# Kernel optimization log

Measured on AMD Instinct MI355X. Metric: run time of the kernel, lower is better.

Reference implementation:

```python
import jax, jax.numpy as jnp
import numpy as np

N, K = 10000, 32          # nodes, max neighbors
NUM_ELEM = 100
D_ATOM = 128              # atom embedding size
D_DIR_IN, D_DIR = 10, 64  # node direction expansion -> embedding
D_DIST_IN, D_DIST = 128, 128  # edge distance expansion -> embedding


def setup_inputs() -> dict:
    key = jax.random.key(0)
    ks = jax.random.split(key, 12)
    inp = {
        "atomic_numbers": jax.random.randint(ks[0], (N,), 0, NUM_ELEM),
        "node_direction_expansion": jax.random.normal(ks[1], (N, D_DIR_IN), jnp.float32),
        "edge_distance_expansion": jax.random.normal(ks[2], (N, K, D_DIST_IN), jnp.float32),
        "neighbor_list": jax.random.randint(ks[3], (N, K), 0, N),
        "neighbor_mask": jax.random.randint(ks[4], (N, K), 0, 2).astype(bool),
        # learned params
        "src_atom_emb": jax.random.uniform(ks[5], (NUM_ELEM, D_ATOM), jnp.float32, -0.001, 0.001),
        "tgt_atom_emb": jax.random.uniform(ks[6], (NUM_ELEM, D_ATOM), jnp.float32, -0.001, 0.001),
        "src_dir_W": jax.random.normal(ks[7], (D_DIR_IN, D_DIR), jnp.float32) * 0.1,
        "src_dir_b": jnp.zeros((D_DIR,), jnp.float32),
        "tgt_dir_W": jax.random.normal(ks[8], (D_DIR_IN, D_DIR), jnp.float32) * 0.1,
        "tgt_dir_b": jnp.zeros((D_DIR,), jnp.float32),
        "dist_W": jax.random.normal(ks[9], (D_DIST_IN, D_DIST), jnp.float32) * 0.1,
        "dist_b": jnp.zeros((D_DIST,), jnp.float32),
    }
    return inp


def reference(atomic_numbers, node_direction_expansion, edge_distance_expansion,
              neighbor_list, neighbor_mask,
              src_atom_emb, tgt_atom_emb,
              src_dir_W, src_dir_b, tgt_dir_W, tgt_dir_b, dist_W, dist_b):
    # per-node embeddings
    sa = src_atom_emb[atomic_numbers]                      # [N, D_ATOM]
    ta = tgt_atom_emb[atomic_numbers]                      # [N, D_ATOM]
    sd = jax.nn.silu(node_direction_expansion @ src_dir_W + src_dir_b)  # [N, D_DIR]
    td = jax.nn.silu(node_direction_expansion @ tgt_dir_W + tgt_dir_b)  # [N, D_DIR]

    # map_sender_receiver_feature: sender gathered via neighbor_list, receiver broadcast
    sender_atom = sa[neighbor_list]                        # [N, K, D_ATOM]
    recv_atom = jnp.broadcast_to(ta[:, None, :], (N, K, D_ATOM))
    sender_dir = sd[neighbor_list]                         # [N, K, D_DIR]
    recv_dir = jnp.broadcast_to(td[:, None, :], (N, K, D_DIR))

    edist = jax.nn.silu(edge_distance_expansion @ dist_W + dist_b)  # [N, K, D_DIST]

    edge_features = jnp.concatenate(
        [edist, sender_dir, sender_atom, recv_dir, recv_atom], axis=-1)  # [N, K, 512]

    # masked mean over neighbors
    m = neighbor_mask.astype(edge_features.dtype)          # [N, K]
    count = m.sum(axis=1, keepdims=True) + 1e-5            # [N, 1]
    out = (edge_features * m[:, :, None]).sum(axis=1) / count  # [N, 512]
    return out
```

## Files before the change

### kernel.cpp

```cpp
#include <hip/hip_runtime.h>
#include <hip/hip_bf16.h>

#define NN 10000
#define KK 32
#define DDIRIN 10
#define DDIR 64
#define DD 128

typedef short bf16x8 __attribute__((ext_vector_type(8)));
typedef float f32x4  __attribute__((ext_vector_type(4)));
typedef float f32x2  __attribute__((ext_vector_type(2)));

__device__ __forceinline__ float silu_f(float x) { return x / (1.0f + __expf(-x)); }

__device__ __forceinline__ ushort2 pk_bf16(float a, float b) {
    __hip_bfloat162 h = __float22bfloat162_rn(float2{a, b});
    union { __hip_bfloat162 h; ushort2 u; } v; v.h = h;
    return v.u;
}

__global__ __launch_bounds__(256) void dirprep_kernel(
    const float* __restrict__ nde,
    const float* __restrict__ sW, const float* __restrict__ sb,
    const float* __restrict__ tW, const float* __restrict__ tb,
    const float* __restrict__ dW,
    float* __restrict__ sd, float* __restrict__ td, ushort* __restrict__ dWb)
{
    int b = blockIdx.x;
    if (b < 32) {
        int v = b * 256 + threadIdx.x;
        int ncol = v >> 6;
        int k0   = (v & 63) * 2;
        ushort2 u = pk_bf16(dW[k0 * DD + ncol], dW[(k0 + 1) * DD + ncol]);
        *reinterpret_cast<ushort2*>(&dWb[ncol * DD + k0]) = u;
        return;
    }
    int gid = (b - 32) * 256 + threadIdx.x;
    int n = gid >> 6, d = gid & 63;
    float a = sb[d], t = tb[d];
    const float* x = nde + n * DDIRIN;
#pragma unroll
    for (int i = 0; i < DDIRIN; ++i) {
        float xv = x[i];
        a = fmaf(xv, sW[i * DDIR + d], a);
        t = fmaf(xv, tW[i * DDIR + d], t);
    }
    sd[gid] = silu_f(a);
    td[gid] = silu_f(t);
}

template<bool PREB>
__global__ __launch_bounds__(256, 2) void gemm_kernel(
    const float* __restrict__ edist,
    const int*   __restrict__ nmask,
    const float* __restrict__ dW,
    const float* __restrict__ db,
    const ushort* __restrict__ dWb,
    float* __restrict__ out)
{
    const int tid  = threadIdx.x;
    const int wid  = tid >> 6;
    const int lane = tid & 63;
    const int l15  = lane & 15;
    const int quad = lane >> 4;
    const int n0   = blockIdx.x * 4;

    __shared__ __align__(16) short s_E[128 * 128];
    __shared__ float s_cnt[4];

    const f32x4* E4 = reinterpret_cast<const f32x4*>(edist + (size_t)n0 * (KK * DD));
    f32x4 va[8], vb[8];
#pragma unroll
    for (int i = 0; i < 8; ++i) {
        int f0 = 2 * tid + 512 * i;
        va[i] = E4[f0];
        vb[i] = E4[f0 + 1];
    }
    const int* nm = nmask + n0 * KK;
    int nmv[8];
#pragma unroll
    for (int i = 0; i < 8; ++i)
        nmv[i] = nm[(tid >> 4) + 16 * i];

    bf16x8 bfrag[2][4];
    float  bias[2];
    if constexpr (PREB) {
#pragma unroll
        for (int c2 = 0; c2 < 2; ++c2) {
            int ncol = (2 * wid + c2) * 16 + l15;
            bias[c2] = db[ncol];
#pragma unroll
            for (int t = 0; t < 4; ++t)
                bfrag[c2][t] = *reinterpret_cast<const bf16x8*>(
                    &dWb[ncol * DD + t * 32 + quad * 8]);
        }
    } else {
#pragma unroll
        for (int c2 = 0; c2 < 2; ++c2) {
            int ncol = (2 * wid + c2) * 16 + l15;
            bias[c2] = db[ncol];
#pragma unroll
            for (int t = 0; t < 4; ++t) {
                bf16x8 v;
#pragma unroll
                for (int j2 = 0; j2 < 4; ++j2) {
                    int k0 = t * 32 + quad * 8 + 2 * j2;
                    ushort2 u = pk_bf16(dW[k0 * DD + ncol], dW[(k0 + 1) * DD + ncol]);
                    v[2 * j2]     = (short)u.x;
                    v[2 * j2 + 1] = (short)u.y;
                }
                bfrag[c2][t] = v;
            }
        }
    }

    if (tid < 4) {
        int c = 0;
#pragma unroll 8
        for (int k = 0; k < KK; ++k) c += (nm[tid * KK + k] != 0) ? 1 : 0;
        s_cnt[tid] = (float)c;
    }

#pragma unroll
    for (int i = 0; i < 8; ++i) {
        int f0  = 2 * tid + 512 * i;
        int row = f0 >> 5;
        f32x4 a = va[i], b = vb[i];
        ushort2 u0 = pk_bf16(a[0], a[1]), u1 = pk_bf16(a[2], a[3]);
        ushort2 u2 = pk_bf16(b[0], b[1]), u3 = pk_bf16(b[2], b[3]);
        bf16x8 v;
        v[0] = (short)u0.x; v[1] = (short)u0.y; v[2] = (short)u1.x; v[3] = (short)u1.y;
        v[4] = (short)u2.x; v[5] = (short)u2.y; v[6] = (short)u3.x; v[7] = (short)u3.y;
        bf16x8 z;
#pragma unroll
        for (int q = 0; q < 8; ++q) z[q] = 0;
        v = (nmv[i] != 0) ? v : z;
        int kb = tid & 15;
        int sw = kb ^ (row & 7);
        *reinterpret_cast<bf16x8*>(&s_E[row * 128 + sw * 8]) = v;
    }
    __syncthreads();

    f32x4 acc[8][2];
#pragma unroll
    for (int rt = 0; rt < 8; ++rt)
#pragma unroll
        for (int c2 = 0; c2 < 2; ++c2)
#pragma unroll
            for (int g = 0; g < 4; ++g) acc[rt][c2][g] = 0.0f;

#pragma unroll
    for (int rt = 0; rt < 8; ++rt) {
        bf16x8 af[4];
        int r = rt * 16 + l15;
#pragma unroll
        for (int t = 0; t < 4; ++t) {
            int kb = (4 * t + quad) ^ (l15 & 7);
            af[t] = *reinterpret_cast<const bf16x8*>(&s_E[r * 128 + kb * 8]);
        }
#pragma unroll
        for (int t = 0; t < 4; ++t) {
            acc[rt][0] = __builtin_amdgcn_mfma_f32_16x16x32_bf16(af[t], bfrag[0][t], acc[rt][0], 0, 0, 0);
            acc[rt][1] = __builtin_amdgcn_mfma_f32_16x16x32_bf16(af[t], bfrag[1][t], acc[rt][1], 0, 0, 0);
        }
    }

#pragma unroll
    for (int c2 = 0; c2 < 2; ++c2) {
        float sbv = silu_f(bias[c2]);
#pragma unroll
        for (int nd = 0; nd < 4; ++nd) {
            float p = 0.0f;
#pragma unroll
            for (int h = 0; h < 2; ++h) {
                int rt = 2 * nd + h;
#pragma unroll
                for (int g = 0; g < 4; ++g)
                    p += silu_f(acc[rt][c2][g] + bias[c2]);
            }
            p += __shfl_xor(p, 16);
            p += __shfl_xor(p, 32);
            if (quad == nd) {
                float c = s_cnt[nd];
                float val = (p - (32.0f - c) * sbv) / (c + 1e-5f);
                out[(size_t)(n0 + nd) * 512 + (2 * wid + c2) * 16 + l15] = val;
            }
        }
    }
}

template<bool USE_WS>
__global__ __launch_bounds__(256) void seg_kernel(
    const int*   __restrict__ an,
    const float* __restrict__ nde,
    const int*   __restrict__ nl,
    const int*   __restrict__ nmask,
    const float* __restrict__ semb,
    const float* __restrict__ temb,
    const float* __restrict__ sW, const float* __restrict__ sb,
    const float* __restrict__ tW, const float* __restrict__ tb,
    const float* __restrict__ sd_ws,
    const float* __restrict__ td_ws,
    float* __restrict__ out)
{
    const int tid  = threadIdx.x;
    const int wid  = tid >> 6;
    const int lane = tid & 63;
    const int n    = blockIdx.x * 4 + wid;

    __shared__ int s_idx[4][KK];
    __shared__ int s_aidx[4][KK];

    int j = 0; bool act = false;
    if (lane < KK) {
        j   = nl[n * KK + lane];
        act = (nmask[n * KK + lane] != 0);
    }
    unsigned long long bits = __ballot(act);
    int cnt = (int)__popcll(bits);
    if (act) {
        int rank = (int)__popcll(bits & ((1ull << lane) - 1ull));
        s_idx[wid][rank]  = j;
        s_aidx[wid][rank] = an[j];
    }
    __syncthreads();

    const float invv  = 1.0f / ((float)cnt + 1e-5f);
    const float scale = (float)cnt * invv;
    float* outn = out + (size_t)n * 512;

    {
        float s = 0.0f;
        if constexpr (USE_WS) {
#pragma unroll 4
            for (int i = 0; i < cnt; ++i)
                s += sd_ws[s_idx[wid][i] * DDIR + lane];
        } else {
            for (int i = 0; i < cnt; ++i) {
                int jj = s_idx[wid][i];
                float a = sb[lane];
#pragma unroll
                for (int q = 0; q < DDIRIN; ++q)
                    a = fmaf(nde[jj * DDIRIN + q], sW[q * DDIR + lane], a);
                s += silu_f(a);
            }
        }
        outn[128 + lane] = s * invv;
    }

    {
        float s0 = 0.0f, s1 = 0.0f;
#pragma unroll 4
        for (int i = 0; i < cnt; ++i) {
            int a = s_aidx[wid][i];
            s0 += semb[a * DD + lane];
            s1 += semb[a * DD + 64 + lane];
        }
        outn[192 + lane] = s0 * invv;
        outn[256 + lane] = s1 * invv;
    }

    {
        float tdv;
        if constexpr (USE_WS) {
            tdv = td_ws[n * DDIR + lane];
        } else {
            float a = tb[lane];
#pragma unroll
            for (int q = 0; q < DDIRIN; ++q)
                a = fmaf(nde[n * DDIRIN + q], tW[q * DDIR + lane], a);
            tdv = silu_f(a);
        }
        outn[320 + lane] = tdv * scale;
    }

    {
        int ann = an[n];
        outn[384 + lane] = temb[ann * DD + lane] * scale;
        outn[448 + lane] = temb[ann * DD + 64 + lane] * scale;
    }
}

extern "C" void kernel_launch(void* const* d_in, const int* in_sizes, int n_in,
                              void* d_out, int out_size, void* d_ws, size_t ws_size,
                              hipStream_t stream) {
    const int*   an    = (const int*)  d_in[0];
    const float* nde   = (const float*)d_in[1];
    const float* edist = (const float*)d_in[2];
    const int*   nl    = (const int*)  d_in[3];
    const int*   nmask = (const int*)  d_in[4];
    const float* semb  = (const float*)d_in[5];
    const float* temb  = (const float*)d_in[6];
    const float* sW    = (const float*)d_in[7];
    const float* sb    = (const float*)d_in[8];
    const float* tW    = (const float*)d_in[9];
    const float* tb    = (const float*)d_in[10];
    const float* dW    = (const float*)d_in[11];
    const float* db    = (const float*)d_in[12];
    float* out = (float*)d_out;

    const size_t dwb_bytes = (size_t)DD * DD * sizeof(ushort);
    const size_t need = dwb_bytes + (size_t)NN * DDIR * sizeof(float) * 2;

    if (ws_size >= need) {
        ushort* dWb = (ushort*)d_ws;
        float*  sd  = (float*)((char*)d_ws + dwb_bytes);
        float*  td  = sd + (size_t)NN * DDIR;
        dirprep_kernel<<<32 + NN * DDIR / 256, 256, 0, stream>>>(
            nde, sW, sb, tW, tb, dW, sd, td, dWb);
        gemm_kernel<true><<<NN / 4, 256, 0, stream>>>(edist, nmask, dW, db, dWb, out);
        seg_kernel<true><<<NN / 4, 256, 0, stream>>>(
            an, nde, nl, nmask, semb, temb, sW, sb, tW, tb, sd, td, out);
    } else {
        gemm_kernel<false><<<NN / 4, 256, 0, stream>>>(edist, nmask, dW, db, nullptr, out);
        seg_kernel<false><<<NN / 4, 256, 0, stream>>>(
            an, nde, nl, nmask, semb, temb, sW, sb, tW, tb, nullptr, nullptr, out);
    }
}
```

Before: 282.6 us.

## Make edge GEMM kernel persistent with register prefetch of next tile

The distance-GEMM kernel becomes a persistent grid-stride loop over 2-node tiles on a fixed 768-block grid. The next tile's fp32 edge rows and mask are loaded into registers while the current tile's MFMAs run, overlapping HBM reads with compute. Neighbor counts now come from a wave ballot and popcount instead of a serial per-thread loop. Shared memory is halved and launch bounds raised to 3 blocks per CU, at the cost of an extra barrier per tile and more register pressure from the prefetch buffers.

```diff
diff --git a/kernel.cpp b/kernel.cpp
--- a/kernel.cpp
+++ b/kernel.cpp
@@ -50,7 +50,7 @@
 }
 
 template<bool PREB>
-__global__ __launch_bounds__(256, 2) void gemm_kernel(
+__global__ __launch_bounds__(256, 3) void gemm_kernel(
     const float* __restrict__ edist,
     const int*   __restrict__ nmask,
     const float* __restrict__ dW,
@@ -63,24 +63,8 @@
     const int lane = tid & 63;
     const int l15  = lane & 15;
     const int quad = lane >> 4;
-    const int n0   = blockIdx.x * 4;
-
-    __shared__ __align__(16) short s_E[128 * 128];
-    __shared__ float s_cnt[4];
-
-    const f32x4* E4 = reinterpret_cast<const f32x4*>(edist + (size_t)n0 * (KK * DD));
-    f32x4 va[8], vb[8];
-#pragma unroll
-    for (int i = 0; i < 8; ++i) {
-        int f0 = 2 * tid + 512 * i;
-        va[i] = E4[f0];
-        vb[i] = E4[f0 + 1];
-    }
-    const int* nm = nmask + n0 * KK;
-    int nmv[8];
-#pragma unroll
-    for (int i = 0; i < 8; ++i)
-        nmv[i] = nm[(tid >> 4) + 16 * i];
+
+    __shared__ __align__(16) short s_E[64 * 128];
 
     bf16x8 bfrag[2][4];
     float  bias[2];
@@ -114,78 +98,111 @@
         }
     }
 
-    if (tid < 4) {
-        int c = 0;
-#pragma unroll 8
-        for (int k = 0; k < KK; ++k) c += (nm[tid * KK + k] != 0) ? 1 : 0;
-        s_cnt[tid] = (float)c;
-    }
-
-#pragma unroll
-    for (int i = 0; i < 8; ++i) {
-        int f0  = 2 * tid + 512 * i;
-        int row = f0 >> 5;
-        f32x4 a = va[i], b = vb[i];
-        ushort2 u0 = pk_bf16(a[0], a[1]), u1 = pk_bf16(a[2], a[3]);
-        ushort2 u2 = pk_bf16(b[0], b[1]), u3 = pk_bf16(b[2], b[3]);
-        bf16x8 v;
-        v[0] = (short)u0.x; v[1] = (short)u0.y; v[2] = (short)u1.x; v[3] = (short)u1.y;
-        v[4] = (short)u2.x; v[5] = (short)u2.y; v[6] = (short)u3.x; v[7] = (short)u3.y;
-        bf16x8 z;
-#pragma unroll
-        for (int q = 0; q < 8; ++q) z[q] = 0;
-        v = (nmv[i] != 0) ? v : z;
-        int kb = tid & 15;
-        int sw = kb ^ (row & 7);
-        *reinterpret_cast<bf16x8*>(&s_E[row * 128 + sw * 8]) = v;
-    }
-    __syncthreads();
-
-    f32x4 acc[8][2];
-#pragma unroll
-    for (int rt = 0; rt < 8; ++rt)
-#pragma unroll
-        for (int c2 = 0; c2 < 2; ++c2)
-#pragma unroll
-            for (int g = 0; g < 4; ++g) acc[rt][c2][g] = 0.0f;
-
-#pragma unroll
-    for (int rt = 0; rt < 8; ++rt) {
-        bf16x8 af[4];
-        int r = rt * 16 + l15;
-#pragma unroll
-        for (int t = 0; t < 4; ++t) {
-            int kb = (4 * t + quad) ^ (l15 & 7);
-            af[t] = *reinterpret_cast<const bf16x8*>(&s_E[r * 128 + kb * 8]);
-        }
-#pragma unroll
-        for (int t = 0; t < 4; ++t) {
-            acc[rt][0] = __builtin_amdgcn_mfma_f32_16x16x32_bf16(af[t], bfrag[0][t], acc[rt][0], 0, 0, 0);
-            acc[rt][1] = __builtin_amdgcn_mfma_f32_16x16x32_bf16(af[t], bfrag[1][t], acc[rt][1], 0, 0, 0);
-        }
-    }
-
-#pragma unroll
-    for (int c2 = 0; c2 < 2; ++c2) {
-        float sbv = silu_f(bias[c2]);
-#pragma unroll
-        for (int nd = 0; nd < 4; ++nd) {
-            float p = 0.0f;
-#pragma unroll
-            for (int h = 0; h < 2; ++h) {
-                int rt = 2 * nd + h;
-#pragma unroll
-                for (int g = 0; g < 4; ++g)
-                    p += silu_f(acc[rt][c2][g] + bias[c2]);
-            }
-            p += __shfl_xor(p, 16);
-            p += __shfl_xor(p, 32);
-            if (quad == nd) {
-                float c = s_cnt[nd];
-                float val = (p - (32.0f - c) * sbv) / (c + 1e-5f);
-                out[(size_t)(n0 + nd) * 512 + (2 * wid + c2) * 16 + l15] = val;
-            }
-        }
+    const int NT     = NN / 2;
+    const int stride = gridDim.x;
+    int tile = blockIdx.x;
+
+    f32x4 va[4], vb[4];
+    int   mval;
+    {
+        const f32x4* E4 = reinterpret_cast<const f32x4*>(edist) + (size_t)tile * 2048;
+#pragma unroll
+        for (int i = 0; i < 4; ++i) {
+            int f0 = 2 * tid + 512 * i;
+            va[i] = E4[f0];
+            vb[i] = E4[f0 + 1];
+        }
+        mval = nmask[tile * 64 + lane];
+    }
+
+    while (true) {
+        const unsigned long long bits = __ballot(mval != 0);
+        const float cnt0 = (float)__popcll(bits & 0xffffffffull);
+        const float cnt1 = (float)__popcll(bits >> 32);
+        const int   n0   = tile * 2;
+
+#pragma unroll
+        for (int i = 0; i < 4; ++i) {
+            int row = (tid >> 4) + 16 * i;
+            f32x4 a = va[i], b = vb[i];
+            ushort2 u0 = pk_bf16(a[0], a[1]), u1 = pk_bf16(a[2], a[3]);
+            ushort2 u2 = pk_bf16(b[0], b[1]), u3 = pk_bf16(b[2], b[3]);
+            bf16x8 v;
+            v[0] = (short)u0.x; v[1] = (short)u0.y; v[2] = (short)u1.x; v[3] = (short)u1.y;
+            v[4] = (short)u2.x; v[5] = (short)u2.y; v[6] = (short)u3.x; v[7] = (short)u3.y;
+            bf16x8 z;
+#pragma unroll
+            for (int q = 0; q < 8; ++q) z[q] = 0;
+            v = ((bits >> row) & 1ull) ? v : z;
+            int kb = tid & 15;
+            int sw = kb ^ (row & 7);
+            *reinterpret_cast<bf16x8*>(&s_E[row * 128 + sw * 8]) = v;
+        }
+        __syncthreads();
+
+        const int  ntile = tile + stride;
+        const bool more  = (ntile < NT);
+        if (more) {
+            const f32x4* E4n = reinterpret_cast<const f32x4*>(edist) + (size_t)ntile * 2048;
+#pragma unroll
+            for (int i = 0; i < 4; ++i) {
+                int f0 = 2 * tid + 512 * i;
+                va[i] = E4n[f0];
+                vb[i] = E4n[f0 + 1];
+            }
+            mval = nmask[ntile * 64 + lane];
+        }
+
+        f32x4 acc[4][2];
+#pragma unroll
+        for (int rt = 0; rt < 4; ++rt)
+#pragma unroll
+            for (int c2 = 0; c2 < 2; ++c2)
+#pragma unroll
+                for (int g = 0; g < 4; ++g) acc[rt][c2][g] = 0.0f;
+
+#pragma unroll
+        for (int rt = 0; rt < 4; ++rt) {
+            bf16x8 af[4];
+            int r = rt * 16 + l15;
+#pragma unroll
+            for (int t = 0; t < 4; ++t) {
+                int kb = (4 * t + quad) ^ (l15 & 7);
+                af[t] = *reinterpret_cast<const bf16x8*>(&s_E[r * 128 + kb * 8]);
+            }
+#pragma unroll
+            for (int t = 0; t < 4; ++t) {
+                acc[rt][0] = __builtin_amdgcn_mfma_f32_16x16x32_bf16(af[t], bfrag[0][t], acc[rt][0], 0, 0, 0);
+                acc[rt][1] = __builtin_amdgcn_mfma_f32_16x16x32_bf16(af[t], bfrag[1][t], acc[rt][1], 0, 0, 0);
+            }
+        }
+
+#pragma unroll
+        for (int c2 = 0; c2 < 2; ++c2) {
+            float sbv = silu_f(bias[c2]);
+#pragma unroll
+            for (int nd = 0; nd < 2; ++nd) {
+                float p = 0.0f;
+#pragma unroll
+                for (int h = 0; h < 2; ++h) {
+                    int rt = 2 * nd + h;
+#pragma unroll
+                    for (int g = 0; g < 4; ++g)
+                        p += silu_f(acc[rt][c2][g] + bias[c2]);
+                }
+                p += __shfl_xor(p, 16);
+                p += __shfl_xor(p, 32);
+                if (quad == nd) {
+                    float c = (nd == 0) ? cnt0 : cnt1;
+                    float val = (p - (32.0f - c) * sbv) / (c + 1e-5f);
+                    out[(size_t)(n0 + nd) * 512 + (2 * wid + c2) * 16 + l15] = val;
+                }
+            }
+        }
+
+        if (!more) break;
+        __syncthreads();
+        tile = ntile;
     }
 }
 
@@ -302,17 +319,19 @@
     const size_t dwb_bytes = (size_t)DD * DD * sizeof(ushort);
     const size_t need = dwb_bytes + (size_t)NN * DDIR * sizeof(float) * 2;
 
+    const int GEMM_GRID = 768;
+
     if (ws_size >= need) {
         ushort* dWb = (ushort*)d_ws;
         float*  sd  = (float*)((char*)d_ws + dwb_bytes);
         float*  td  = sd + (size_t)NN * DDIR;
         dirprep_kernel<<<32 + NN * DDIR / 256, 256, 0, stream>>>(
             nde, sW, sb, tW, tb, dW, sd, td, dWb);
-        gemm_kernel<true><<<NN / 4, 256, 0, stream>>>(edist, nmask, dW, db, dWb, out);
+        gemm_kernel<true><<<GEMM_GRID, 256, 0, stream>>>(edist, nmask, dW, db, dWb, out);
         seg_kernel<true><<<NN / 4, 256, 0, stream>>>(
             an, nde, nl, nmask, semb, temb, sW, sb, tW, tb, sd, td, out);
     } else {
-        gemm_kernel<false><<<NN / 4, 256, 0, stream>>>(edist, nmask, dW, db, nullptr, out);
+        gemm_kernel<false><<<GEMM_GRID, 256, 0, stream>>>(edist, nmask, dW, db, nullptr, out);
         seg_kernel<false><<<NN / 4, 256, 0, stream>>>(
             an, nde, nl, nmask, semb, temb, sW, sb, tW, tb, nullptr, nullptr, out);
     }
```

Result: no change. 283.8 us (+0.4%).
